# Kernel optimization log

Hardware: AMD Instinct MI355X
Metric: run time of the kernel (lower is better)

## Reference

```python
import jax, jax.numpy as jnp
import numpy as np

B, S, E = 8, 2048, 512

def setup_inputs() -> dict:
    key = jax.random.key(0)
    ks = jax.random.split(key, 7)
    Q = jax.random.normal(ks[0], (B, S, E), dtype=jnp.float32)
    K = jax.random.normal(ks[1], (B, S, E), dtype=jnp.float32)
    pad_mask = jax.random.randint(ks[2], (B, S, S), 0, 2).astype(bool)
    # torch nn.Linear weights are [out, in]; y = x @ W.T + b
    sc = 1.0 / np.sqrt(E)
    Wq = jax.random.uniform(ks[3], (E, E), jnp.float32, -sc, sc)
    Wk = jax.random.uniform(ks[4], (E, E), jnp.float32, -sc, sc)
    Wv = jax.random.uniform(ks[5], (E, E), jnp.float32, -sc, sc)
    Wp = jax.random.uniform(ks[6], (E, E), jnp.float32, -sc, sc)
    bp = jnp.zeros((E,), jnp.float32)
    return {"Q": Q, "K": K, "pad_mask": pad_mask, "Wq": Wq, "Wk": Wk, "Wv": Wv, "Wp": Wp, "bp": bp}

def reference(Q, K, pad_mask, Wq, Wk, Wv, Wp, bp):
    scale = E ** (-0.5)
    V = K  # V aliases K before projection, as in the original
    q = jnp.einsum('bse,fe->bsf', Q, Wq)   # q_map (no bias)
    k = jnp.einsum('bse,fe->bsf', K, Wk)   # k_map
    v = jnp.einsum('bse,fe->bsf', V, Wv)   # v_map
    scores = jnp.einsum('bqe,bke->bqk', q, k) * scale  # [B,S,S]
    scores = jnp.where(pad_mask, -1e9, scores)
    attn = jax.nn.softmax(scores, axis=-1)
    out = jnp.einsum('bqk,bke->bqe', attn, v)
    out = jnp.einsum('bse,fe->bsf', out, Wp) + bp       # proj
    return q + out  # residual uses projected Q (faithful to source)
```

## Files before the change

kernel.cpp:

```cpp
#include <hip/hip_runtime.h>
#include <hip/hip_bf16.h>

typedef short v8s __attribute__((ext_vector_type(8)));
typedef float v4f __attribute__((ext_vector_type(4)));

static constexpr int BB = 8, SS = 2048, EE = 512;

enum { EPI_BF16 = 0, EPI_SCALE = 1, EPI_FINAL = 2 };

struct EpiParams {
  float scale;
  const float* bias;
  const __hip_bfloat16* resid;
  int resid_ld;
};

static constexpr int SMEM_BYTES = 34816;

struct CastParams {
  const float* src[4];
  __hip_bfloat16* dst[4];
};

__global__ __launch_bounds__(256) void cast_weights(CastParams cp) {
  const int seg = blockIdx.x >> 7;
  const int b = blockIdx.x & 127;
  const float* x = cp.src[seg] + (unsigned long long)b * 2048;
  __hip_bfloat16* y = cp.dst[seg] + (unsigned long long)b * 2048;
  int i = threadIdx.x * 8;
  float4 f0 = ((const float4*)(x + i))[0];
  float4 f1 = ((const float4*)(x + i))[1];
  alignas(16) __hip_bfloat16 h[8];
  h[0] = __float2bfloat16(f0.x); h[1] = __float2bfloat16(f0.y);
  h[2] = __float2bfloat16(f0.z); h[3] = __float2bfloat16(f0.w);
  h[4] = __float2bfloat16(f1.x); h[5] = __float2bfloat16(f1.y);
  h[6] = __float2bfloat16(f1.z); h[7] = __float2bfloat16(f1.w);
  *(uint4*)(y + i) = *(uint4*)h;
}

__device__ __forceinline__ void stage_tile64(const __hip_bfloat16* __restrict__ G,
                                             int row0, int ld, int k0,
                                             __hip_bfloat16* lds, int wave, int lane) {
#pragma unroll
  for (int t = 0; t < 4; ++t) {
    const int p = (wave * 4 + t) * 64 + lane;
    const int row = p >> 3;
    const int g = (p & 7) ^ (row & 7);
    const __hip_bfloat16* src = G + (unsigned long long)(row0 + row) * ld + k0 + g * 8;
    __builtin_amdgcn_global_load_lds(
        (const __attribute__((address_space(1))) void*)src,
        (__attribute__((address_space(3))) void*)(lds + (wave * 4 + t) * 512),
        16, 0, 0);
  }
}

__device__ __forceinline__ void stage_tile64_f32(const float* __restrict__ G,
                                                 int row0, int ld, int k0,
                                                 __hip_bfloat16* lds, int tid) {
#pragma unroll
  for (int c = 0; c < 4; ++c) {
    const int p = c * 256 + tid;
    const int row = p >> 3;
    const int g = (p & 7) ^ (row & 7);
    const float* src = G + (unsigned long long)(row0 + row) * ld + k0 + g * 8;
    float4 f0 = ((const float4*)src)[0];
    float4 f1 = ((const float4*)src)[1];
    alignas(16) __hip_bfloat16 h[8];
    h[0] = __float2bfloat16(f0.x); h[1] = __float2bfloat16(f0.y);
    h[2] = __float2bfloat16(f0.z); h[3] = __float2bfloat16(f0.w);
    h[4] = __float2bfloat16(f1.x); h[5] = __float2bfloat16(f1.y);
    h[6] = __float2bfloat16(f1.z); h[7] = __float2bfloat16(f1.w);
    *(uint4*)&lds[p * 8] = *(uint4*)h;
  }
}

template <int EPI, bool AF32, bool BF32>
__device__ __forceinline__ void gemm_body(const void* Agv, const void* Bgv,
                                          void* Cg, int K, int lda, int ldb, int ldc,
                                          int m0, int n0, const EpiParams& ep,
                                          unsigned char* smem) {
  __hip_bfloat16* As = (__hip_bfloat16*)smem;
  __hip_bfloat16* Bs = As + 128 * 64;

  const int tid = threadIdx.x;
  const int lane = tid & 63;
  const int wave = tid >> 6;
  const int wr = wave >> 1;
  const int wc = wave & 1;

  v4f acc[4][4];
  const v4f vzero = {0.f, 0.f, 0.f, 0.f};
#pragma unroll
  for (int i = 0; i < 4; ++i)
#pragma unroll
    for (int j = 0; j < 4; ++j) acc[i][j] = vzero;

  const int fr = lane & 15;
  const int fq = lane >> 4;

  for (int k0 = 0; k0 < K; k0 += 64) {
    __syncthreads();
    if constexpr (AF32)
      stage_tile64_f32((const float*)Agv, m0, lda, k0, As, tid);
    else
      stage_tile64((const __hip_bfloat16*)Agv, m0, lda, k0, As, wave, lane);
    if constexpr (BF32)
      stage_tile64_f32((const float*)Bgv, n0, ldb, k0, Bs, tid);
    else
      stage_tile64((const __hip_bfloat16*)Bgv, n0, ldb, k0, Bs, wave, lane);
    __syncthreads();

#pragma unroll
    for (int ks = 0; ks < 2; ++ks) {
      const int gq = ks * 4 + fq;
      v8s a[4], b[4];
#pragma unroll
      for (int i = 0; i < 4; ++i) {
        const int r = wr * 64 + i * 16 + fr;
        a[i] = *(const v8s*)&As[r * 64 + ((gq ^ (r & 7)) * 8)];
      }
#pragma unroll
      for (int j = 0; j < 4; ++j) {
        const int r = wc * 64 + j * 16 + fr;
        b[j] = *(const v8s*)&Bs[r * 64 + ((gq ^ (r & 7)) * 8)];
      }
#pragma unroll
      for (int i = 0; i < 4; ++i)
#pragma unroll
        for (int j = 0; j < 4; ++j)
          acc[i][j] = __builtin_amdgcn_mfma_f32_16x16x32_bf16(a[i], b[j], acc[i][j], 0, 0, 0);
    }
  }

  const int cf = lane & 15;
  const int rq = (lane >> 4) * 4;

  __syncthreads();

  if constexpr (EPI != EPI_FINAL) {
    __hip_bfloat16* Ct = (__hip_bfloat16*)smem;
    const int ST = 136;
#pragma unroll
    for (int i = 0; i < 4; ++i) {
      const int rl = wr * 64 + i * 16 + rq;
#pragma unroll
      for (int j = 0; j < 4; ++j) {
        const int col = wc * 64 + j * 16 + cf;
#pragma unroll
        for (int r = 0; r < 4; ++r) {
          float v = acc[i][j][r];
          if constexpr (EPI == EPI_SCALE) v *= ep.scale;
          Ct[(rl + r) * ST + col] = __float2bfloat16(v);
        }
      }
    }
    __syncthreads();
    __hip_bfloat16* C = (__hip_bfloat16*)Cg;
#pragma unroll
    for (int c = 0; c < 8; ++c) {
      const int idx = c * 256 + tid;
      const int row = idx >> 4;
      const int colc = (idx & 15) * 8;
      *(v8s*)&C[(unsigned long long)(m0 + row) * ldc + n0 + colc] =
          *(const v8s*)&Ct[row * ST + colc];
    }
  } else {
    float* Cf = (float*)smem;
    const int ST = 132;
    float* C = (float*)Cg;
#pragma unroll
    for (int h = 0; h < 2; ++h) {
      if (wr == h) {
#pragma unroll
        for (int i = 0; i < 4; ++i) {
          const int rl = i * 16 + rq;
#pragma unroll
          for (int j = 0; j < 4; ++j) {
            const int col = wc * 64 + j * 16 + cf;
#pragma unroll
            for (int r = 0; r < 4; ++r) Cf[(rl + r) * ST + col] = acc[i][j][r];
          }
        }
      }
      __syncthreads();
#pragma unroll
      for (int c = 0; c < 8; ++c) {
        const int idx = c * 256 + tid;
        const int row = idx >> 5;
        const int colc = (idx & 31) * 4;
        const int grow = m0 + h * 64 + row;
        const int gcol = n0 + colc;
        float4 v = *(const float4*)&Cf[row * ST + colc];
        float4 b4 = *(const float4*)&ep.bias[gcol];
        ushort4 r4 = *(const ushort4*)&ep.resid[(unsigned long long)grow * ep.resid_ld + gcol];
        v.x += b4.x + __bfloat162float(*(__hip_bfloat16*)&r4.x);
        v.y += b4.y + __bfloat162float(*(__hip_bfloat16*)&r4.y);
        v.z += b4.z + __bfloat162float(*(__hip_bfloat16*)&r4.z);
        v.w += b4.w + __bfloat162float(*(__hip_bfloat16*)&r4.w);
        *(float4*)&C[(unsigned long long)grow * ldc + gcol] = v;
      }
      if (h == 0) __syncthreads();
    }
  }
}

template <int EPI>
__global__ __launch_bounds__(256, 3) void gemm_bt(
    const __hip_bfloat16* __restrict__ Ag, const __hip_bfloat16* __restrict__ Bg,
    void* __restrict__ Cg, int K, int lda, int ldb, int ldc,
    unsigned long long sAz, unsigned long long sBz, unsigned long long sCz, EpiParams ep) {
  __shared__ __align__(16) unsigned char smem[SMEM_BYTES];
  const unsigned long long z = blockIdx.z;
  void* Cz;
  if constexpr (EPI == EPI_FINAL) Cz = (void*)((float*)Cg + z * sCz);
  else Cz = (void*)((__hip_bfloat16*)Cg + z * sCz);
  gemm_body<EPI, false, false>(Ag + z * sAz, Bg + z * sBz, Cz, K, lda, ldb, ldc,
                               blockIdx.y * 128, blockIdx.x * 128, ep, smem);
}

__global__ __launch_bounds__(256, 3) void gemm_qkv(
    const float* __restrict__ Q, const float* __restrict__ K,
    const __hip_bfloat16* __restrict__ Wq, const __hip_bfloat16* __restrict__ Wk,
    const __hip_bfloat16* __restrict__ Wv,
    __hip_bfloat16* __restrict__ qb, __hip_bfloat16* __restrict__ kb,
    __hip_bfloat16* __restrict__ vT) {
  __shared__ __align__(16) unsigned char smem[SMEM_BYTES];
  const int z = blockIdx.z;
  EpiParams ep{};
  if (z == 2) {
    gemm_body<EPI_BF16, false, true>(Wv, K, vT, EE, EE, EE, BB * SS,
                                     blockIdx.y * 128, blockIdx.x * 128, ep, smem);
  } else {
    const float* A = (z == 0) ? Q : K;
    const __hip_bfloat16* B = (z == 0) ? Wq : Wk;
    __hip_bfloat16* C = (z == 0) ? qb : kb;
    gemm_body<EPI_BF16, true, false>(A, B, C, EE, EE, EE, EE,
                                     blockIdx.x * 128, blockIdx.y * 128, ep, smem);
  }
}

static constexpr int FLASH_LDS = 149248;

__device__ __forceinline__ void stage_K64(const __hip_bfloat16* __restrict__ Kb, int kv0,
                                          __hip_bfloat16* lds, int tid) {
  const int wv = tid >> 6;
#pragma unroll
  for (int c = 0; c < 8; ++c) {
    const int p = c * 512 + tid;
    const int chunk = p >> 9;
    const int row = (p >> 3) & 63;
    const int g = (p & 7) ^ (row & 7);
    const __hip_bfloat16* src = Kb + (unsigned long long)(kv0 + row) * 512ull + chunk * 64 + g * 8;
    __builtin_amdgcn_global_load_lds(
        (const __attribute__((address_space(1))) void*)src,
        (__attribute__((address_space(3))) void*)(lds + (c * 512 + wv * 64) * 8),
        16, 0, 0);
  }
}

__global__ __launch_bounds__(512, 2) void flash_attn(
    const __hip_bfloat16* __restrict__ qb, const __hip_bfloat16* __restrict__ kb,
    const __hip_bfloat16* __restrict__ vT, const unsigned char* __restrict__ mask,
    __hip_bfloat16* __restrict__ ob) {
  extern __shared__ __align__(16) char fsm[];
  __hip_bfloat16* Ks0 = (__hip_bfloat16*)fsm;
  __hip_bfloat16* Ps0 = Ks0 + 2 * 32768;
  float* m_s   = (float*)(fsm + 147456);
  float* l_s   = m_s + 64;
  float* fac_s = l_s + 64;
  float* pmax  = fac_s + 64;
  float* psum  = pmax + 128;

  const int tid = threadIdx.x;
  const int lane = tid & 63;
  const int w = tid >> 6;
  const int fr = lane & 15;
  const int fq = lane >> 4;
  const int wq = w & 3;
  const int wk = w >> 2;
  const int b = blockIdx.x & 7;
  const int q0 = (blockIdx.x >> 3) * 64;
  const unsigned long long bS = (unsigned long long)b * 2048ull;
  const float SC = 0.044194173824159216f;

  v8s qf[16];
  {
    const __hip_bfloat16* qrow = qb + (bS + q0 + wq * 16 + fr) * 512ull;
#pragma unroll
    for (int kk = 0; kk < 16; ++kk) qf[kk] = *(const v8s*)&qrow[kk * 32 + fq * 8];
  }

  v4f acc[4][4];
  const v4f vz = {0.f, 0.f, 0.f, 0.f};
#pragma unroll
  for (int i = 0; i < 4; ++i)
#pragma unroll
    for (int j = 0; j < 4; ++j) acc[i][j] = vz;

  if (tid < 64) { m_s[tid] = -1e30f; l_s[tid] = 0.f; }

  const __hip_bfloat16* Kb = kb + bS * 512ull;
  stage_K64(Kb, 0, Ks0, tid);
  __syncthreads();

  for (int t = 0; t < 32; ++t) {
    __hip_bfloat16* KsT = Ks0 + (t & 1) * 32768;
    __hip_bfloat16* PsT = Ps0 + (t & 1) * 4096;
    if (t < 31) stage_K64(Kb, (t + 1) * 64, Ks0 + ((t + 1) & 1) * 32768, tid);

    const int kv0 = t * 64;

    unsigned char mk[2][4];
#pragma unroll
    for (int j = 0; j < 2; ++j)
#pragma unroll
      for (int r = 0; r < 4; ++r)
        mk[j][r] = mask[(bS + q0 + wq * 16 + fq * 4 + r) * 2048ull + kv0 + wk * 32 + j * 16 + fr];

    v4f sa[2] = {vz, vz};
    __builtin_amdgcn_s_setprio(1);
#pragma unroll
    for (int kk = 0; kk < 16; ++kk) {
#pragma unroll
      for (int j = 0; j < 2; ++j) {
        const int rr = wk * 32 + j * 16 + fr;
        v8s kf = *(const v8s*)&KsT[(kk >> 1) * 4096 + rr * 64 + ((((kk & 1) * 4 + fq) ^ (rr & 7)) * 8)];
        sa[j] = __builtin_amdgcn_mfma_f32_16x16x32_bf16(qf[kk], kf, sa[j], 0, 0, 0);
      }
    }
    __builtin_amdgcn_s_setprio(0);

    float sv[2][4];
    float rmx[4] = {-3e38f, -3e38f, -3e38f, -3e38f};
#pragma unroll
    for (int j = 0; j < 2; ++j)
#pragma unroll
      for (int r = 0; r < 4; ++r) {
        const float x = mk[j][r] ? -1e9f : sa[j][r] * SC;
        sv[j][r] = x;
        rmx[r] = fmaxf(rmx[r], x);
      }
#pragma unroll
    for (int off = 1; off <= 8; off <<= 1)
#pragma unroll
      for (int r = 0; r < 4; ++r) rmx[r] = fmaxf(rmx[r], __shfl_xor(rmx[r], off));
    if (fr == 0)
      *(float4*)&pmax[wk * 64 + wq * 16 + fq * 4] = make_float4(rmx[0], rmx[1], rmx[2], rmx[3]);
    __syncthreads();

    if (tid < 64) {
      const float mo = m_s[tid];
      const float mn = fmaxf(mo, fmaxf(pmax[tid], pmax[64 + tid]));
      m_s[tid] = mn;
      fac_s[tid] = __expf(mo - mn);
    }
    __syncthreads();

    float4 mn4 = *(const float4*)&m_s[wq * 16 + fq * 4];
    const float mnr[4] = {mn4.x, mn4.y, mn4.z, mn4.w};
    float rsm[4] = {0.f, 0.f, 0.f, 0.f};
#pragma unroll
    for (int j = 0; j < 2; ++j) {
      const int col = wk * 32 + j * 16 + fr;
      const int cg = col >> 3, cl = col & 7;
#pragma unroll
      for (int r = 0; r < 4; ++r) {
        const float p = __expf(sv[j][r] - mnr[r]);
        rsm[r] += p;
        const int row = wq * 16 + fq * 4 + r;
        PsT[row * 64 + ((cg ^ (row & 7)) * 8) + cl] = __float2bfloat16(p);
      }
    }
#pragma unroll
    for (int off = 1; off <= 8; off <<= 1)
#pragma unroll
      for (int r = 0; r < 4; ++r) rsm[r] += __shfl_xor(rsm[r], off);
    if (fr == 0)
      *(float4*)&psum[wk * 64 + wq * 16 + fq * 4] = make_float4(rsm[0], rsm[1], rsm[2], rsm[3]);
#pragma unroll
    for (int i = 0; i < 4; ++i) {
      const float4 f4 = *(const float4*)&fac_s[i * 16 + fq * 4];
      const float fv[4] = {f4.x, f4.y, f4.z, f4.w};
#pragma unroll
      for (int j = 0; j < 4; ++j)
#pragma unroll
        for (int r = 0; r < 4; ++r) acc[i][j][r] *= fv[r];
    }
    __syncthreads();

    if (tid < 64) l_s[tid] = l_s[tid] * fac_s[tid] + psum[tid] + psum[64 + tid];

    __builtin_amdgcn_s_setprio(1);
#pragma unroll
    for (int ks = 0; ks < 2; ++ks) {
      v8s pa[4], vb[4];
#pragma unroll
      for (int i = 0; i < 4; ++i) {
        const int row = i * 16 + fr;
        pa[i] = *(const v8s*)&PsT[row * 64 + (((ks * 4 + fq) ^ (row & 7)) * 8)];
      }
#pragma unroll
      for (int j = 0; j < 4; ++j)
        vb[j] = *(const v8s*)&vT[(unsigned long long)(w * 64 + j * 16 + fr) * 16384ull +
                                 bS + kv0 + ks * 32 + fq * 8];
#pragma unroll
      for (int i = 0; i < 4; ++i)
#pragma unroll
        for (int j = 0; j < 4; ++j)
          acc[i][j] = __builtin_amdgcn_mfma_f32_16x16x32_bf16(pa[i], vb[j], acc[i][j], 0, 0, 0);
    }
    __builtin_amdgcn_s_setprio(0);
  }

  __syncthreads();
#pragma unroll
  for (int i = 0; i < 4; ++i) {
    const float4 l4 = *(const float4*)&l_s[i * 16 + fq * 4];
    const float inv[4] = {1.f / l4.x, 1.f / l4.y, 1.f / l4.z, 1.f / l4.w};
#pragma unroll
    for (int r = 0; r < 4; ++r) {
      __hip_bfloat16* orow = ob + (bS + q0 + i * 16 + fq * 4 + r) * 512ull + w * 64 + fr;
#pragma unroll
      for (int j = 0; j < 4; ++j)
        orow[j * 16] = __float2bfloat16(acc[i][j][r] * inv[r]);
    }
  }
}

extern "C" void kernel_launch(void* const* d_in, const int* in_sizes, int n_in,
                              void* d_out, int out_size, void* d_ws, size_t ws_size,
                              hipStream_t stream) {
  const float* Q = (const float*)d_in[0];
  const float* K = (const float*)d_in[1];
  const unsigned char* mask = (const unsigned char*)d_in[2];
  const float* Wq = (const float*)d_in[3];
  const float* Wk = (const float*)d_in[4];
  const float* Wv = (const float*)d_in[5];
  const float* Wp = (const float*)d_in[6];
  const float* bp = (const float*)d_in[7];
  float* out = (float*)d_out;

  char* ws = (char*)d_ws;
  const unsigned long long MB = 1024ull * 1024ull;
  __hip_bfloat16* qb = (__hip_bfloat16*)(ws + 0 * MB);
  __hip_bfloat16* kb = (__hip_bfloat16*)(ws + 16 * MB);
  __hip_bfloat16* vT = (__hip_bfloat16*)(ws + 32 * MB);
  __hip_bfloat16* Wqb = (__hip_bfloat16*)(ws + 48 * MB);
  __hip_bfloat16* Wkb = Wqb + 512 * 512;
  __hip_bfloat16* Wvb = Wkb + 512 * 512;
  __hip_bfloat16* Wpb = Wvb + 512 * 512;
  __hip_bfloat16* ob = (__hip_bfloat16*)(ws + 64 * MB);

  dim3 blk(256, 1, 1);

  CastParams cp;
  cp.src[0] = Wq; cp.dst[0] = Wqb;
  cp.src[1] = Wk; cp.dst[1] = Wkb;
  cp.src[2] = Wv; cp.dst[2] = Wvb;
  cp.src[3] = Wp; cp.dst[3] = Wpb;
  cast_weights<<<dim3(512, 1, 1), blk, 0, stream>>>(cp);

  gemm_qkv<<<dim3((BB * SS) / 128, EE / 128, 3), blk, 0, stream>>>(
      Q, K, Wqb, Wkb, Wvb, qb, kb, vT);

  static bool attr_done = false;
  if (!attr_done) {
    hipFuncSetAttribute((const void*)flash_attn,
                        hipFuncAttributeMaxDynamicSharedMemorySize, FLASH_LDS);
    attr_done = true;
  }
  flash_attn<<<dim3(256, 1, 1), dim3(512, 1, 1), FLASH_LDS, stream>>>(
      qb, kb, vT, mask, ob);

  EpiParams epf{};
  epf.bias = bp;
  epf.resid = qb;
  epf.resid_ld = EE;
  gemm_bt<EPI_FINAL><<<dim3(EE / 128, (BB * SS) / 128, 1), blk, 0, stream>>>(
      ob, Wpb, out, EE, EE, EE, EE, 0ull, 0ull, 0ull, epf);
}
```

Before: 413.1 us.

## Prefetch mask tiles and V fragments, fold softmax max update into all warps

Mask bytes are staged into LDS with async global-to-LDS copies, double-buffered alongside K, instead of being read as scattered per-thread byte loads. V fragments are loaded at the top of the iteration so their global latency overlaps the QK MFMAs. The separate single-wave running-max step and its extra barrier are removed: every wave computes the new max and rescale factors redundantly from a double-buffered m_s. This adds a barrier at the end of each iteration, uses a single P buffer, and holds more V registers live, which risks extra register pressure.

```diff
diff --git a/kernel.cpp b/kernel.cpp
--- a/kernel.cpp
+++ b/kernel.cpp
@@ -258,18 +258,31 @@
   }
 }
 
+__device__ __forceinline__ void stage_mask(const unsigned char* __restrict__ Mb, int kv0,
+                                           unsigned char* lds, int tid) {
+  if (tid < 256) {
+    const int row = tid >> 2;
+    const int g = tid & 3;
+    const unsigned char* src = Mb + (unsigned long long)row * 2048ull + kv0 + g * 16;
+    __builtin_amdgcn_global_load_lds(
+        (const __attribute__((address_space(1))) void*)src,
+        (__attribute__((address_space(3))) void*)(lds + tid * 16),
+        16, 0, 0);
+  }
+}
+
 __global__ __launch_bounds__(512, 2) void flash_attn(
     const __hip_bfloat16* __restrict__ qb, const __hip_bfloat16* __restrict__ kb,
     const __hip_bfloat16* __restrict__ vT, const unsigned char* __restrict__ mask,
     __hip_bfloat16* __restrict__ ob) {
   extern __shared__ __align__(16) char fsm[];
   __hip_bfloat16* Ks0 = (__hip_bfloat16*)fsm;
-  __hip_bfloat16* Ps0 = Ks0 + 2 * 32768;
-  float* m_s   = (float*)(fsm + 147456);
-  float* l_s   = m_s + 64;
-  float* fac_s = l_s + 64;
-  float* pmax  = fac_s + 64;
-  float* psum  = pmax + 128;
+  __hip_bfloat16* Ps  = (__hip_bfloat16*)(fsm + 131072);
+  unsigned char* Msk  = (unsigned char*)(fsm + 139264);
+  float* m_s  = (float*)(fsm + 147456);
+  float* l_s  = (float*)(fsm + 147968);
+  float* pmax = (float*)(fsm + 148224);
+  float* psum = (float*)(fsm + 148736);
 
   const int tid = threadIdx.x;
   const int lane = tid & 63;
@@ -300,22 +313,28 @@
   if (tid < 64) { m_s[tid] = -1e30f; l_s[tid] = 0.f; }
 
   const __hip_bfloat16* Kb = kb + bS * 512ull;
+  const unsigned char* Mb = mask + (bS + q0) * 2048ull;
   stage_K64(Kb, 0, Ks0, tid);
+  stage_mask(Mb, 0, Msk, tid);
   __syncthreads();
 
   for (int t = 0; t < 32; ++t) {
     __hip_bfloat16* KsT = Ks0 + (t & 1) * 32768;
-    __hip_bfloat16* PsT = Ps0 + (t & 1) * 4096;
-    if (t < 31) stage_K64(Kb, (t + 1) * 64, Ks0 + ((t + 1) & 1) * 32768, tid);
-
+    const unsigned char* mskT = Msk + (t & 1) * 4096;
     const int kv0 = t * 64;
 
-    unsigned char mk[2][4];
-#pragma unroll
-    for (int j = 0; j < 2; ++j)
-#pragma unroll
-      for (int r = 0; r < 4; ++r)
-        mk[j][r] = mask[(bS + q0 + wq * 16 + fq * 4 + r) * 2048ull + kv0 + wk * 32 + j * 16 + fr];
+    if (t < 31) {
+      stage_K64(Kb, (t + 1) * 64, Ks0 + ((t + 1) & 1) * 32768, tid);
+      stage_mask(Mb, (t + 1) * 64, Msk + ((t + 1) & 1) * 4096, tid);
+    }
+
+    v8s vb[2][4];
+#pragma unroll
+    for (int ks = 0; ks < 2; ++ks)
+#pragma unroll
+      for (int j = 0; j < 4; ++j)
+        vb[ks][j] = *(const v8s*)&vT[(unsigned long long)(w * 64 + j * 16 + fr) * 16384ull +
+                                     bS + kv0 + ks * 32 + fq * 8];
 
     v4f sa[2] = {vz, vz};
     __builtin_amdgcn_s_setprio(1);
@@ -333,31 +352,54 @@
     float sv[2][4];
     float rmx[4] = {-3e38f, -3e38f, -3e38f, -3e38f};
 #pragma unroll
-    for (int j = 0; j < 2; ++j)
+    for (int j = 0; j < 2; ++j) {
+      const int col = wk * 32 + j * 16 + fr;
 #pragma unroll
       for (int r = 0; r < 4; ++r) {
-        const float x = mk[j][r] ? -1e9f : sa[j][r] * SC;
+        const unsigned char mk = mskT[(wq * 16 + fq * 4 + r) * 64 + col];
+        const float x = mk ? -1e9f : sa[j][r] * SC;
         sv[j][r] = x;
         rmx[r] = fmaxf(rmx[r], x);
       }
+    }
 #pragma unroll
     for (int off = 1; off <= 8; off <<= 1)
 #pragma unroll
       for (int r = 0; r < 4; ++r) rmx[r] = fmaxf(rmx[r], __shfl_xor(rmx[r], off));
     if (fr == 0)
       *(float4*)&pmax[wk * 64 + wq * 16 + fq * 4] = make_float4(rmx[0], rmx[1], rmx[2], rmx[3]);
-    __syncthreads();
-
-    if (tid < 64) {
-      const float mo = m_s[tid];
-      const float mn = fmaxf(mo, fmaxf(pmax[tid], pmax[64 + tid]));
-      m_s[tid] = mn;
-      fac_s[tid] = __expf(mo - mn);
-    }
-    __syncthreads();
-
-    float4 mn4 = *(const float4*)&m_s[wq * 16 + fq * 4];
-    const float mnr[4] = {mn4.x, mn4.y, mn4.z, mn4.w};
+
+    asm volatile("s_waitcnt lgkmcnt(0)" ::: "memory");
+    __builtin_amdgcn_s_barrier();
+    __builtin_amdgcn_sched_barrier(0);
+
+    const float* mo_cur = m_s + (t & 1) * 64;
+    float* mo_nxt = m_s + ((t + 1) & 1) * 64;
+    float mnr[4];
+#pragma unroll
+    for (int i = 0; i < 4; ++i) {
+      const int r0 = i * 16 + fq * 4;
+      float4 mo4 = *(const float4*)&mo_cur[r0];
+      float4 p04 = *(const float4*)&pmax[r0];
+      float4 p14 = *(const float4*)&pmax[64 + r0];
+      float mn[4], fc[4];
+      mn[0] = fmaxf(mo4.x, fmaxf(p04.x, p14.x));
+      mn[1] = fmaxf(mo4.y, fmaxf(p04.y, p14.y));
+      mn[2] = fmaxf(mo4.z, fmaxf(p04.z, p14.z));
+      mn[3] = fmaxf(mo4.w, fmaxf(p04.w, p14.w));
+      fc[0] = __expf(mo4.x - mn[0]);
+      fc[1] = __expf(mo4.y - mn[1]);
+      fc[2] = __expf(mo4.z - mn[2]);
+      fc[3] = __expf(mo4.w - mn[3]);
+#pragma unroll
+      for (int j = 0; j < 4; ++j)
+#pragma unroll
+        for (int r = 0; r < 4; ++r) acc[i][j][r] *= fc[r];
+      if (i == wq) { mnr[0] = mn[0]; mnr[1] = mn[1]; mnr[2] = mn[2]; mnr[3] = mn[3]; }
+      if (w == 0 && fr == 0)
+        *(float4*)&mo_nxt[r0] = make_float4(mn[0], mn[1], mn[2], mn[3]);
+    }
+
     float rsm[4] = {0.f, 0.f, 0.f, 0.f};
 #pragma unroll
     for (int j = 0; j < 2; ++j) {
@@ -368,7 +410,7 @@
         const float p = __expf(sv[j][r] - mnr[r]);
         rsm[r] += p;
         const int row = wq * 16 + fq * 4 + r;
-        PsT[row * 64 + ((cg ^ (row & 7)) * 8) + cl] = __float2bfloat16(p);
+        Ps[row * 64 + ((cg ^ (row & 7)) * 8) + cl] = __float2bfloat16(p);
       }
     }
 #pragma unroll
@@ -377,42 +419,39 @@
       for (int r = 0; r < 4; ++r) rsm[r] += __shfl_xor(rsm[r], off);
     if (fr == 0)
       *(float4*)&psum[wk * 64 + wq * 16 + fq * 4] = make_float4(rsm[0], rsm[1], rsm[2], rsm[3]);
-#pragma unroll
-    for (int i = 0; i < 4; ++i) {
-      const float4 f4 = *(const float4*)&fac_s[i * 16 + fq * 4];
-      const float fv[4] = {f4.x, f4.y, f4.z, f4.w};
-#pragma unroll
-      for (int j = 0; j < 4; ++j)
-#pragma unroll
-        for (int r = 0; r < 4; ++r) acc[i][j][r] *= fv[r];
-    }
-    __syncthreads();
-
-    if (tid < 64) l_s[tid] = l_s[tid] * fac_s[tid] + psum[tid] + psum[64 + tid];
+
+    asm volatile("s_waitcnt lgkmcnt(0)" ::: "memory");
+    __builtin_amdgcn_s_barrier();
+    __builtin_amdgcn_sched_barrier(0);
+
+    if (tid < 64) {
+      const float mo = mo_cur[tid];
+      const float mn = fmaxf(mo, fmaxf(pmax[tid], pmax[64 + tid]));
+      l_s[tid] = l_s[tid] * __expf(mo - mn) + psum[tid] + psum[64 + tid];
+    }
 
     __builtin_amdgcn_s_setprio(1);
 #pragma unroll
     for (int ks = 0; ks < 2; ++ks) {
-      v8s pa[4], vb[4];
+      v8s pa[4];
 #pragma unroll
       for (int i = 0; i < 4; ++i) {
         const int row = i * 16 + fr;
-        pa[i] = *(const v8s*)&PsT[row * 64 + (((ks * 4 + fq) ^ (row & 7)) * 8)];
-      }
-#pragma unroll
-      for (int j = 0; j < 4; ++j)
-        vb[j] = *(const v8s*)&vT[(unsigned long long)(w * 64 + j * 16 + fr) * 16384ull +
-                                 bS + kv0 + ks * 32 + fq * 8];
+        pa[i] = *(const v8s*)&Ps[row * 64 + (((ks * 4 + fq) ^ (row & 7)) * 8)];
+      }
 #pragma unroll
       for (int i = 0; i < 4; ++i)
 #pragma unroll
         for (int j = 0; j < 4; ++j)
-          acc[i][j] = __builtin_amdgcn_mfma_f32_16x16x32_bf16(pa[i], vb[j], acc[i][j], 0, 0, 0);
+          acc[i][j] = __builtin_amdgcn_mfma_f32_16x16x32_bf16(pa[i], vb[ks][j], acc[i][j], 0, 0, 0);
     }
     __builtin_amdgcn_s_setprio(0);
-  }
-
-  __syncthreads();
+
+    asm volatile("s_waitcnt vmcnt(0) lgkmcnt(0)" ::: "memory");
+    __builtin_amdgcn_s_barrier();
+    __builtin_amdgcn_sched_barrier(0);
+  }
+
 #pragma unroll
   for (int i = 0; i < 4; ++i) {
     const float4 l4 = *(const float4*)&l_s[i * 16 + fq * 4];
```

After: 428.3 us. 3.7% more time.
